# Kernel tuning notes

Hardware: AMD Instinct MI355X
Metric: run time of the kernel (lower is better)

Reference implementation:

```python
import jax, jax.numpy as jnp
import numpy as np

T, B, IN, H = 2048, 2048, 5, 10


def setup_inputs() -> dict:
    key = jax.random.key(0)
    ks = jax.random.split(key, 7)
    return {
        "x": jax.random.normal(ks[0], (T, B, IN), dtype=jnp.float32),
        "hx0": jax.random.uniform(ks[1], (B, H), dtype=jnp.float32),
        "cx0": jax.random.uniform(ks[2], (B, H), dtype=jnp.float32),
        "W_ih": jax.random.normal(ks[3], (4 * H, IN), dtype=jnp.float32) * 0.3,
        "W_hh": jax.random.normal(ks[4], (4 * H, H), dtype=jnp.float32) * 0.3,
        "b_ih": jax.random.normal(ks[5], (4 * H,), dtype=jnp.float32) * 0.1,
        "b_hh": jax.random.normal(ks[6], (4 * H,), dtype=jnp.float32) * 0.1,
    }


def reference(x, hx0, cx0, W_ih, W_hh, b_ih, b_hh):
    # torch.nn.LSTMCell gate order: i, f, g, o
    bias = b_ih + b_hh  # [4H]

    def step(carry, xt):
        h, c = carry  # [B, H] each
        gates = xt @ W_ih.T + h @ W_hh.T + bias  # [B, 4H]
        i, f, g, o = jnp.split(gates, 4, axis=-1)
        c_new = jax.nn.sigmoid(f) * c + jax.nn.sigmoid(i) * jnp.tanh(g)
        h_new = jax.nn.sigmoid(o) * jnp.tanh(c_new)
        return (h_new, c_new), h_new

    _, hs = jax.lax.scan(step, (hx0, cx0), x)  # hs: [T, B, H]
    # original concatenates per-step hx along dim 0 -> [T*B, H]
    return hs.reshape(-1, hs.shape[-1])
```

## Files before the change

### kernel.cpp

```cpp
#include <hip/hip_runtime.h>


#define T_STEPS 2048
#define BATCH   2048
#define NIN     5
#define NH      10
#define PF      8
#define GPW     6

typedef float v2f __attribute__((ext_vector_type(2)));

__device__ __forceinline__ float hw_exp2(float v) { return __builtin_amdgcn_exp2f(v); }
__device__ __forceinline__ float hw_rcp(float v)  { return __builtin_amdgcn_rcpf(v); }
__device__ __forceinline__ float bperm_f(int srclane, float v) {
    return __builtin_bit_cast(float,
        __builtin_amdgcn_ds_bpermute(srclane << 2, __builtin_bit_cast(int, v)));
}
__device__ __forceinline__ v2f splat2(float v) { v2f r; r.x = v; r.y = v; return r; }

__global__ __launch_bounds__(64) void lstm_fused_kernel(
    const float* __restrict__ x,   const float* __restrict__ hx0,
    const float* __restrict__ cx0, const float* __restrict__ Wih,
    const float* __restrict__ Whh, const float* __restrict__ bih,
    const float* __restrict__ bhh, float* __restrict__ out)
{
    const float L2E  = 1.4426950408889634f;
    const float L2E2 = 2.8853900817779268f;

    const int lane = threadIdx.x;
    int grp = lane / NH;
    if (grp > GPW - 1) grp = GPW - 1;
    int j = lane - grp * NH;
    if (j > NH - 1) j = NH - 1;

    const int b    = blockIdx.x * GPW + grp;
    const bool bval = (lane < GPW * NH) && (b < BATCH);
    const int bl   = (b < BATCH) ? b : (BATCH - 1);

    const int ri = j, rf = NH + j, rg = 2 * NH + j, ro = 3 * NH + j;

    v2f wxif[NIN], wxgo[NIN], whif[NH], whgo[NH];
#pragma unroll
    for (int k = 0; k < NIN; ++k) {
        wxif[k].x = Wih[ri * NIN + k];  wxif[k].y = Wih[rf * NIN + k];
        wxgo[k].x = Wih[rg * NIN + k];  wxgo[k].y = Wih[ro * NIN + k];
    }
#pragma unroll
    for (int k = 0; k < NH; ++k) {
        whif[k].x = Whh[ri * NH + k];   whif[k].y = Whh[rf * NH + k];
        whgo[k].x = Whh[rg * NH + k];   whgo[k].y = Whh[ro * NH + k];
    }
    v2f bif, bgo;
    bif.x = bih[ri] + bhh[ri];  bif.y = bih[rf] + bhh[rf];
    bgo.x = bih[rg] + bhh[rg];  bgo.y = bih[ro] + bhh[ro];

    float hv[NH];
#pragma unroll
    for (int k = 0; k < NH; ++k) hv[k] = hx0[bl * NH + k];
    float cst = cx0[bl * NH + j];

    const int srcbase = grp * NH;

    const float* xb = x + (size_t)bl * NIN;
    float xr[PF][NIN];
#pragma unroll
    for (int q = 0; q < PF; ++q)
#pragma unroll
        for (int k = 0; k < NIN; ++k)
            xr[q][k] = xb[(size_t)q * (BATCH * NIN) + k];

    float* outp = out + (size_t)bl * NH + j;

#pragma unroll 1
    for (int t0 = 0; t0 < T_STEPS; t0 += PF) {
#pragma unroll
        for (int q = 0; q < PF; ++q) {
            const int t = t0 + q;

            v2f aif0 = bif, ago0 = bgo;
            v2f aif1 = splat2(0.0f), ago1 = splat2(0.0f);
            {
                v2f xx0 = splat2(xr[q][0]);
                v2f xx1 = splat2(xr[q][1]);
                v2f xx2 = splat2(xr[q][2]);
                v2f xx3 = splat2(xr[q][3]);
                v2f xx4 = splat2(xr[q][4]);
                aif0 += xx0 * wxif[0];  ago0 += xx0 * wxgo[0];
                aif1 += xx1 * wxif[1];  ago1 += xx1 * wxgo[1];
                aif0 += xx2 * wxif[2];  ago0 += xx2 * wxgo[2];
                aif1 += xx3 * wxif[3];  ago1 += xx3 * wxgo[3];
                aif0 += xx4 * wxif[4];  ago0 += xx4 * wxgo[4];
            }

            {
                int tn = t + PF;
                if (tn > T_STEPS - 1) tn = T_STEPS - 1;
#pragma unroll
                for (int k = 0; k < NIN; ++k)
                    xr[q][k] = xb[(size_t)tn * (BATCH * NIN) + k];
            }

#pragma unroll
            for (int k = 0; k < NH; k += 2) {
                v2f h0 = splat2(hv[k]);
                v2f h1 = splat2(hv[k + 1]);
                aif0 += h0 * whif[k];      ago0 += h0 * whgo[k];
                aif1 += h1 * whif[k + 1];  ago1 += h1 * whgo[k + 1];
            }
            const v2f aif = aif0 + aif1;
            const v2f ago = ago0 + ago1;

            const float si = hw_rcp(1.0f + hw_exp2(-L2E  * aif.x));
            const float sf = hw_rcp(1.0f + hw_exp2(-L2E  * aif.y));
            const float tg = fmaf(2.0f, hw_rcp(1.0f + hw_exp2(-L2E2 * ago.x)), -1.0f);
            const float so = hw_rcp(1.0f + hw_exp2(-L2E  * ago.y));

            cst = fmaf(sf, cst, si * tg);
            const float tc = fmaf(2.0f, hw_rcp(1.0f + hw_exp2(-L2E2 * cst)), -1.0f);
            const float h  = so * tc;

            if (bval) outp[(size_t)t * (BATCH * NH)] = h;

#pragma unroll
            for (int k = 0; k < NH; ++k)
                hv[k] = bperm_f(srcbase + k, h);
        }
    }
}

extern "C" void kernel_launch(void* const* d_in, const int* in_sizes, int n_in,
                              void* d_out, int out_size, void* d_ws, size_t ws_size,
                              hipStream_t stream) {
    const float* x   = (const float*)d_in[0];
    const float* hx0 = (const float*)d_in[1];
    const float* cx0 = (const float*)d_in[2];
    const float* Wih = (const float*)d_in[3];
    const float* Whh = (const float*)d_in[4];
    const float* bih = (const float*)d_in[5];
    const float* bhh = (const float*)d_in[6];
    float* out = (float*)d_out;

    const int nblocks = (BATCH + GPW - 1) / GPW;
    lstm_fused_kernel<<<nblocks, 64, 0, stream>>>(x, hx0, cx0, Wih, Whh, bih, bhh, out);
}
```

Measured before the change: 766.6 us.

## Replace ds_bpermute hidden-state broadcast with DPP row rotations over 16-lane rows

Each batch element now occupies one 16-lane DPP row, four per wavefront instead of six, and the hidden state is exchanged with row_ror DPP moves instead of ten ds_bpermute LDS-path shuffles per step. The recurrent weights are pre-rotated per lane into 16 slots, with zeros in the padding slots, so the rotated h values line up with the right weights. This removes LDS-crossbar latency from the serial per-step dependency chain. In exchange, fewer batch elements fit per wave, so more blocks are launched, and each step does 16 multiply-add slots where 10 were needed before.

```diff
diff --git a/kernel.cpp b/kernel.cpp
--- a/kernel.cpp
+++ b/kernel.cpp
@@ -6,17 +6,20 @@
 #define NIN     5
 #define NH      10
 #define PF      8
-#define GPW     6
+#define GPW     4
 
 typedef float v2f __attribute__((ext_vector_type(2)));
 
 __device__ __forceinline__ float hw_exp2(float v) { return __builtin_amdgcn_exp2f(v); }
 __device__ __forceinline__ float hw_rcp(float v)  { return __builtin_amdgcn_rcpf(v); }
-__device__ __forceinline__ float bperm_f(int srclane, float v) {
+__device__ __forceinline__ v2f splat2(float v) { v2f r; r.x = v; r.y = v; return r; }
+
+template<int CTRL>
+__device__ __forceinline__ float dpp_f(float v) {
+    int i = __builtin_bit_cast(int, v);
     return __builtin_bit_cast(float,
-        __builtin_amdgcn_ds_bpermute(srclane << 2, __builtin_bit_cast(int, v)));
+        __builtin_amdgcn_update_dpp(i, i, CTRL, 0xF, 0xF, false));
 }
-__device__ __forceinline__ v2f splat2(float v) { v2f r; r.x = v; r.y = v; return r; }
 
 __global__ __launch_bounds__(64) void lstm_fused_kernel(
     const float* __restrict__ x,   const float* __restrict__ hx0,
@@ -28,40 +31,41 @@
     const float L2E2 = 2.8853900817779268f;
 
     const int lane = threadIdx.x;
-    int grp = lane / NH;
-    if (grp > GPW - 1) grp = GPW - 1;
-    int j = lane - grp * NH;
-    if (j > NH - 1) j = NH - 1;
+    const int row  = lane >> 4;
+    const int j    = lane & 15;
+    const int b    = blockIdx.x * GPW + row;
+    const int jc   = (j < NH) ? j : (NH - 1);
+    const bool act = (j < NH);
 
-    const int b    = blockIdx.x * GPW + grp;
-    const bool bval = (lane < GPW * NH) && (b < BATCH);
-    const int bl   = (b < BATCH) ? b : (BATCH - 1);
+    const int ri = jc, rf = NH + jc, rg = 2 * NH + jc, ro = 3 * NH + jc;
 
-    const int ri = j, rf = NH + j, rg = 2 * NH + j, ro = 3 * NH + j;
-
-    v2f wxif[NIN], wxgo[NIN], whif[NH], whgo[NH];
+    v2f wxif[NIN], wxgo[NIN];
 #pragma unroll
     for (int k = 0; k < NIN; ++k) {
         wxif[k].x = Wih[ri * NIN + k];  wxif[k].y = Wih[rf * NIN + k];
         wxgo[k].x = Wih[rg * NIN + k];  wxgo[k].y = Wih[ro * NIN + k];
     }
-#pragma unroll
-    for (int k = 0; k < NH; ++k) {
-        whif[k].x = Whh[ri * NH + k];   whif[k].y = Whh[rf * NH + k];
-        whgo[k].x = Whh[rg * NH + k];   whgo[k].y = Whh[ro * NH + k];
-    }
     v2f bif, bgo;
     bif.x = bih[ri] + bhh[ri];  bif.y = bih[rf] + bhh[rf];
     bgo.x = bih[rg] + bhh[rg];  bgo.y = bih[ro] + bhh[ro];
 
-    float hv[NH];
+    v2f whif_s[16], whgo_s[16];
 #pragma unroll
-    for (int k = 0; k < NH; ++k) hv[k] = hx0[bl * NH + k];
-    float cst = cx0[bl * NH + j];
+    for (int s = 0; s < 16; ++s) {
+        const int u = (j - s) & 15;
+        if (u < NH) {
+            whif_s[s].x = Whh[ri * NH + u];  whif_s[s].y = Whh[rf * NH + u];
+            whgo_s[s].x = Whh[rg * NH + u];  whgo_s[s].y = Whh[ro * NH + u];
+        } else {
+            whif_s[s] = splat2(0.0f);
+            whgo_s[s] = splat2(0.0f);
+        }
+    }
 
-    const int srcbase = grp * NH;
+    float h   = hx0[b * NH + jc];
+    float cst = cx0[b * NH + jc];
 
-    const float* xb = x + (size_t)bl * NIN;
+    const float* xb = x + (size_t)b * NIN;
     float xr[PF][NIN];
 #pragma unroll
     for (int q = 0; q < PF; ++q)
@@ -69,7 +73,7 @@
         for (int k = 0; k < NIN; ++k)
             xr[q][k] = xb[(size_t)q * (BATCH * NIN) + k];
 
-    float* outp = out + (size_t)bl * NH + j;
+    float* outp = out + (size_t)b * NH + j;
 
 #pragma unroll 1
     for (int t0 = 0; t0 < T_STEPS; t0 += PF) {
@@ -77,19 +81,20 @@
         for (int q = 0; q < PF; ++q) {
             const int t = t0 + q;
 
-            v2f aif0 = bif, ago0 = bgo;
-            v2f aif1 = splat2(0.0f), ago1 = splat2(0.0f);
+            v2f a0 = bif,          g0 = bgo;
+            v2f a1 = splat2(0.f),  g1 = splat2(0.f);
+            v2f a2 = splat2(0.f),  g2 = splat2(0.f);
+            v2f a3 = splat2(0.f),  g3 = splat2(0.f);
+
             {
-                v2f xx0 = splat2(xr[q][0]);
-                v2f xx1 = splat2(xr[q][1]);
-                v2f xx2 = splat2(xr[q][2]);
-                v2f xx3 = splat2(xr[q][3]);
-                v2f xx4 = splat2(xr[q][4]);
-                aif0 += xx0 * wxif[0];  ago0 += xx0 * wxgo[0];
-                aif1 += xx1 * wxif[1];  ago1 += xx1 * wxgo[1];
-                aif0 += xx2 * wxif[2];  ago0 += xx2 * wxgo[2];
-                aif1 += xx3 * wxif[3];  ago1 += xx3 * wxgo[3];
-                aif0 += xx4 * wxif[4];  ago0 += xx4 * wxgo[4];
+                v2f x0 = splat2(xr[q][0]), x1 = splat2(xr[q][1]),
+                    x2 = splat2(xr[q][2]), x3 = splat2(xr[q][3]),
+                    x4 = splat2(xr[q][4]);
+                a0 += x0 * wxif[0];  g0 += x0 * wxgo[0];
+                a1 += x1 * wxif[1];  g1 += x1 * wxgo[1];
+                a2 += x2 * wxif[2];  g2 += x2 * wxgo[2];
+                a3 += x3 * wxif[3];  g3 += x3 * wxgo[3];
+                a0 += x4 * wxif[4];  g0 += x4 * wxgo[4];
             }
 
             {
@@ -100,15 +105,27 @@
                     xr[q][k] = xb[(size_t)tn * (BATCH * NIN) + k];
             }
 
+            float r0 = h;
+            float r1 = dpp_f<0x124>(h);
+            float r2 = dpp_f<0x128>(h);
+            float r3 = dpp_f<0x12C>(h);
 #pragma unroll
-            for (int k = 0; k < NH; k += 2) {
-                v2f h0 = splat2(hv[k]);
-                v2f h1 = splat2(hv[k + 1]);
-                aif0 += h0 * whif[k];      ago0 += h0 * whgo[k];
-                aif1 += h1 * whif[k + 1];  ago1 += h1 * whgo[k + 1];
+            for (int s = 0; s < 4; ++s) {
+                v2f h0 = splat2(r0), h1 = splat2(r1),
+                    h2 = splat2(r2), h3 = splat2(r3);
+                a0 += h0 * whif_s[s];       g0 += h0 * whgo_s[s];
+                a1 += h1 * whif_s[s + 4];   g1 += h1 * whgo_s[s + 4];
+                a2 += h2 * whif_s[s + 8];   g2 += h2 * whgo_s[s + 8];
+                a3 += h3 * whif_s[s + 12];  g3 += h3 * whgo_s[s + 12];
+                if (s < 3) {
+                    r0 = dpp_f<0x121>(r0);
+                    r1 = dpp_f<0x121>(r1);
+                    r2 = dpp_f<0x121>(r2);
+                    r3 = dpp_f<0x121>(r3);
+                }
             }
-            const v2f aif = aif0 + aif1;
-            const v2f ago = ago0 + ago1;
+            const v2f aif = (a0 + a1) + (a2 + a3);
+            const v2f ago = (g0 + g1) + (g2 + g3);
 
             const float si = hw_rcp(1.0f + hw_exp2(-L2E  * aif.x));
             const float sf = hw_rcp(1.0f + hw_exp2(-L2E  * aif.y));
@@ -117,13 +134,9 @@
 
             cst = fmaf(sf, cst, si * tg);
             const float tc = fmaf(2.0f, hw_rcp(1.0f + hw_exp2(-L2E2 * cst)), -1.0f);
-            const float h  = so * tc;
+            h = so * tc;
 
-            if (bval) outp[(size_t)t * (BATCH * NH)] = h;
-
-#pragma unroll
-            for (int k = 0; k < NH; ++k)
-                hv[k] = bperm_f(srcbase + k, h);
+            if (act) outp[(size_t)t * (BATCH * NH)] = h;
         }
     }
 }
@@ -140,6 +153,6 @@
     const float* bhh = (const float*)d_in[6];
     float* out = (float*)d_out;
 
-    const int nblocks = (BATCH + GPW - 1) / GPW;
+    const int nblocks = BATCH / GPW;
     lstm_fused_kernel<<<nblocks, 64, 0, stream>>>(x, hx0, cx0, Wih, Whh, bih, bhh, out);
 }
```

Result: slower. 939.8 us (+22.6%).
